# Performance work log

Hardware: AMD Instinct MI355X
Metric: run time of the kernel (lower is better)

## Reference

```python
import jax, jax.numpy as jnp
import numpy as np


def setup_inputs() -> dict:
    key = jax.random.key(0)
    ks = jax.random.split(key, 8)
    B, C, H, W = 4, 512, 64, 64
    O = 64  # output_size for f/g projections
    x = jax.random.normal(ks[0], (B, C, H, W), dtype=jnp.float32)
    s = 0.02
    f_w = jax.random.normal(ks[1], (O, C), dtype=jnp.float32) * s
    f_b = jnp.zeros((O,), dtype=jnp.float32)
    g_w = jax.random.normal(ks[2], (O, C), dtype=jnp.float32) * s
    g_b = jnp.zeros((O,), dtype=jnp.float32)
    h_w = jax.random.normal(ks[3], (C, C), dtype=jnp.float32) * s
    h_b = jnp.zeros((C,), dtype=jnp.float32)
    gamma = jnp.float32(0.5)  # torch init is 0.0; nonzero to exercise the attention path
    return {"x": x, "f_w": f_w, "f_b": f_b, "g_w": g_w, "g_b": g_b,
            "h_w": h_w, "h_b": h_b, "gamma": gamma}


def reference(x, f_w, f_b, g_w, g_b, h_w, h_b, gamma):
    B, C, Hh, Ww = x.shape
    N = Hh * Ww
    # 1x1 convs == per-pixel linear projections
    xf = x.reshape(B, C, N)                                   # [B,C,N]
    f = jnp.einsum('oc,bcn->bon', f_w, xf) + f_b[None, :, None]  # [B,O,N]
    g = jnp.einsum('oc,bcn->bon', g_w, xf) + g_b[None, :, None]  # [B,O,N]
    h = jnp.einsum('oc,bcn->bon', h_w, xf) + h_b[None, :, None]  # [B,C,N]
    # scores[b,i,j] = <f[:, i], g[:, j]>  (f transposed to [B,N,O] then bmm with g)
    scores = jnp.einsum('boi,boj->bij', f, g)                 # [B,N,N]
    # NOTE: original uses nn.Softmax(dim=1) -> normalize over the i (first N) axis
    sm = jax.nn.softmax(scores, axis=1)                       # [B,N,N]
    attn = jnp.einsum('bcn,bnm->bcm', h, sm)                  # [B,C,N]
    out = gamma * attn.reshape(B, C, Hh, Ww) + x
    return out
```

## Files before the change

### kernel.cpp

```cpp
#include <hip/hip_runtime.h>


#define N_PIX 4096
#define C_IN  512

typedef __attribute__((ext_vector_type(8)))  short bf16x8;
typedef __attribute__((ext_vector_type(16))) float f32x16;

typedef __attribute__((address_space(1))) const unsigned int guint;
typedef __attribute__((address_space(3))) unsigned int luint;

__device__ __forceinline__ void gload_lds16(const void* g, void* l) {
    __builtin_amdgcn_global_load_lds((guint*)g, (luint*)l, 16, 0, 0);
}

__device__ inline unsigned int f2bf(float f) {
    union { float f; unsigned u; } x; x.f = f;
    unsigned r = x.u + 0x7FFFu + ((x.u >> 16) & 1u);
    return r >> 16;
}

__device__ __forceinline__ unsigned cvt_pk_bf16(float a, float b) {
#if __has_builtin(__builtin_amdgcn_cvt_pk_bf16_f32)
    auto r = __builtin_amdgcn_cvt_pk_bf16_f32(a, b);
    unsigned u; __builtin_memcpy(&u, &r, 4); return u;
#else
    return f2bf(a) | (f2bf(b) << 16);
#endif
}

__device__ __forceinline__ unsigned pk_fp8x4(float a, float b, float c, float d) {
    int v = 0;
    v = __builtin_amdgcn_cvt_pk_fp8_f32(a, b, v, false);
    v = __builtin_amdgcn_cvt_pk_fp8_f32(c, d, v, true);
    return (unsigned)v;
}

__global__ __launch_bounds__(256) void pack_w(
    const float* __restrict__ f_w, const float* __restrict__ g_w,
    const float* __restrict__ h_w, unsigned short* __restrict__ wall)
{
    __shared__ __align__(16) unsigned short Ls[32 * 520];
    const int t  = threadIdx.x;
    const int tt = blockIdx.x;
    const float* W; int rbase;
    if (tt < 2)      { W = f_w; rbase = tt * 32; }
    else if (tt < 4) { W = g_w; rbase = (tt - 2) * 32; }
    else             { W = h_w; rbase = (tt - 4) * 32; }

    #pragma unroll
    for (int k = 0; k < 16; ++k) {
        const int off = (t + k * 256) * 4;
        const int row = off >> 9, col = off & 511;
        float4 v = *(const float4*)&W[(size_t)(rbase + row) * C_IN + col];
        uint2 pk; pk.x = cvt_pk_bf16(v.x, v.y); pk.y = cvt_pk_bf16(v.z, v.w);
        *(uint2*)&Ls[row * 520 + col] = pk;
    }
    __syncthreads();
    #pragma unroll
    for (int j = 0; j < 8; ++j) {
        const int o = t + j * 256;
        const int q = o >> 6, lq = o & 63;
        const int row = lq & 31, c0 = q * 16 + (lq >> 5) * 8;
        uint4 pk = *(const uint4*)&Ls[row * 520 + c0];
        *(uint4*)&wall[(size_t)tt * 16384 + (size_t)o * 8] = pk;
    }
}

__global__ __launch_bounds__(512, 4) void proj_kernel(
    const float* __restrict__ x,
    const unsigned short* __restrict__ wall,
    const float* __restrict__ f_b, const float* __restrict__ g_b,
    const float* __restrict__ h_b,
    unsigned short* __restrict__ fa, unsigned short* __restrict__ gbuf,
    unsigned char* __restrict__ ha)
{
    __shared__ __align__(16) unsigned short Xf[2][8192];
    const int t    = threadIdx.x;
    const int w    = t >> 6;
    const int l    = t & 63;
    const int half = l >> 5;
    const int tx = t & 15;
    const int ty = t >> 4;
    const int c0 = ty * 2;
    const int qs = c0 >> 4;
    const int woff = (c0 & 7);
    const int hfs = (c0 >> 3) & 1;

    const int blk = blockIdx.x;

    if (blk < 256) {
        const int b  = blk >> 6;
        const int nb = blk & 63;
        const int n0g = nb * 64;
        const int n0 = tx * 4;

        f32x16 acc[2][2];
        #pragma unroll
        for (int j = 0; j < 2; ++j)
            #pragma unroll
            for (int s = 0; s < 2; ++s)
                #pragma unroll
                for (int r = 0; r < 16; ++r) acc[j][s][r] = 0.f;

        const unsigned short* wp0 = wall + (size_t)(4 + w * 2) * 16384 + (size_t)l * 8;
        const unsigned short* wp1 = wp0 + 16384;
        bf16x8 wc0 = *(const bf16x8*)wp0;
        bf16x8 wc1 = *(const bf16x8*)wp1;

        float4 v0 = *(const float4*)&x[((size_t)(b * C_IN + c0)) * N_PIX + n0g + n0];
        float4 v1 = *(const float4*)&x[((size_t)(b * C_IN + c0 + 1)) * N_PIX + n0g + n0];

        for (int it = 0; it < 8; ++it) {
            {
                unsigned short* xb = &Xf[it & 1][0];
                const float a0[4] = {v0.x, v0.y, v0.z, v0.w};
                const float a1[4] = {v1.x, v1.y, v1.z, v1.w};
                #pragma unroll
                for (int j = 0; j < 4; ++j) {
                    const int n = n0 + j;
                    const int off = ((n >> 5) * 4 + qs) * 512
                                  + ((n & 31) + 32 * hfs) * 8 + woff;
                    *(unsigned*)&xb[off] = cvt_pk_bf16(a0[j], a1[j]);
                }
            }
            if (it < 7) {
                v0 = *(const float4*)&x[((size_t)(b * C_IN + (it + 1) * 64 + c0)) * N_PIX + n0g + n0];
                v1 = *(const float4*)&x[((size_t)(b * C_IN + (it + 1) * 64 + c0 + 1)) * N_PIX + n0g + n0];
            }
            __syncthreads();
            const unsigned short* xb = &Xf[it & 1][0];
            #pragma unroll
            for (int q = 0; q < 4; ++q) {
                const int qn = (it * 4 + q + 1) & 31;
                bf16x8 wn0 = *(const bf16x8*)(wp0 + (size_t)qn * 512);
                bf16x8 wn1 = *(const bf16x8*)(wp1 + (size_t)qn * 512);
                bf16x8 x0 = *(const bf16x8*)&xb[(0 * 4 + q) * 512 + l * 8];
                bf16x8 x1 = *(const bf16x8*)&xb[(1 * 4 + q) * 512 + l * 8];
                acc[0][0] = __builtin_amdgcn_mfma_f32_32x32x16_bf16(x0, wc0, acc[0][0], 0, 0, 0);
                acc[0][1] = __builtin_amdgcn_mfma_f32_32x32x16_bf16(x1, wc0, acc[0][1], 0, 0, 0);
                acc[1][0] = __builtin_amdgcn_mfma_f32_32x32x16_bf16(x0, wc1, acc[1][0], 0, 0, 0);
                acc[1][1] = __builtin_amdgcn_mfma_f32_32x32x16_bf16(x1, wc1, acc[1][1], 0, 0, 0);
                wc0 = wn0; wc1 = wn1;
            }
            __syncthreads();
        }

        #pragma unroll
        for (int j = 0; j < 2; ++j) {
            const int ctile = w * 2 + j;
            const float hb = h_b[ctile * 32 + (l & 31)];
            #pragma unroll
            for (int ns = 0; ns < 2; ++ns) {
                const int ntile = nb * 2 + ns;
                #pragma unroll
                for (int j2 = 0; j2 < 4; ++j2) {
                    const int q  = ntile * 2 + (j2 >> 1);
                    const int lp = (l & 31) + 32 * (j2 & 1);
                    unsigned pk = pk_fp8x4(acc[j][ns][4 * j2 + 0] + hb,
                                           acc[j][ns][4 * j2 + 1] + hb,
                                           acc[j][ns][4 * j2 + 2] + hb,
                                           acc[j][ns][4 * j2 + 3] + hb);
                    size_t off = (((size_t)(b * 16 + ctile) * 256 + q) * 64 + lp) * 8 + 4 * half;
                    *(unsigned*)&ha[off] = pk;
                }
            }
        }
    } else {
        const int blk2 = blk - 256;
        const int b   = blk2 >> 5;
        const int nb2 = blk2 & 31;
        const int n0g = nb2 * 128;
        const int tt    = w & 3;
        const int npair = w >> 2;

        f32x16 acc[2];
        #pragma unroll
        for (int s = 0; s < 2; ++s)
            #pragma unroll
            for (int r = 0; r < 16; ++r) acc[s][r] = 0.f;

        const unsigned short* wpf = wall + (size_t)tt * 16384 + (size_t)l * 8;
        bf16x8 wcf = *(const bf16x8*)wpf;

        float4 v00 = *(const float4*)&x[((size_t)(b * C_IN + c0)) * N_PIX + n0g + tx * 4];
        float4 v10 = *(const float4*)&x[((size_t)(b * C_IN + c0 + 1)) * N_PIX + n0g + tx * 4];
        float4 v01 = *(const float4*)&x[((size_t)(b * C_IN + c0)) * N_PIX + n0g + 64 + tx * 4];
        float4 v11 = *(const float4*)&x[((size_t)(b * C_IN + c0 + 1)) * N_PIX + n0g + 64 + tx * 4];

        for (int it = 0; it < 8; ++it) {
            {
                unsigned short* xb = &Xf[it & 1][0];
                const float a00[4] = {v00.x, v00.y, v00.z, v00.w};
                const float a10[4] = {v10.x, v10.y, v10.z, v10.w};
                const float a01[4] = {v01.x, v01.y, v01.z, v01.w};
                const float a11[4] = {v11.x, v11.y, v11.z, v11.w};
                #pragma unroll
                for (int j = 0; j < 4; ++j) {
                    const int n = tx * 4 + j;
                    const int off0 = ((n >> 5) * 4 + qs) * 512
                                   + ((n & 31) + 32 * hfs) * 8 + woff;
                    *(unsigned*)&xb[off0] = cvt_pk_bf16(a00[j], a10[j]);
                    const int n2 = 64 + n;
                    const int off1 = ((n2 >> 5) * 4 + qs) * 512
                                   + ((n2 & 31) + 32 * hfs) * 8 + woff;
                    *(unsigned*)&xb[off1] = cvt_pk_bf16(a01[j], a11[j]);
                }
            }
            if (it < 7) {
                const size_t rb = (size_t)(b * C_IN + (it + 1) * 64 + c0) * N_PIX + n0g;
                v00 = *(const float4*)&x[rb + tx * 4];
                v10 = *(const float4*)&x[rb + N_PIX + tx * 4];
                v01 = *(const float4*)&x[rb + 64 + tx * 4];
                v11 = *(const float4*)&x[rb + N_PIX + 64 + tx * 4];
            }
            __syncthreads();
            const unsigned short* xb = &Xf[it & 1][0];
            #pragma unroll
            for (int q = 0; q < 4; ++q) {
                const int qn = (it * 4 + q + 1) & 31;
                bf16x8 wnf = *(const bf16x8*)(wpf + (size_t)qn * 512);
                bf16x8 x0 = *(const bf16x8*)&xb[((npair * 2 + 0) * 4 + q) * 512 + l * 8];
                bf16x8 x1 = *(const bf16x8*)&xb[((npair * 2 + 1) * 4 + q) * 512 + l * 8];
                acc[0] = __builtin_amdgcn_mfma_f32_32x32x16_bf16(wcf, x0, acc[0], 0, 0, 0);
                acc[1] = __builtin_amdgcn_mfma_f32_32x32x16_bf16(wcf, x1, acc[1], 0, 0, 0);
                wcf = wnf;
            }
            __syncthreads();
        }

        unsigned short* buf = (tt < 2) ? fa : gbuf;
        const float* bias = (tt < 2) ? f_b : g_b;
        #pragma unroll
        for (int s = 0; s < 2; ++s) {
            const int ntile = nb2 * 4 + npair * 2 + s;
            #pragma unroll
            for (int j2 = 0; j2 < 4; ++j2) {
                const int o_base = (tt & 1) * 32 + 8 * j2 + 4 * half;
                float4 bv = *(const float4*)&bias[o_base];
                const int q  = o_base >> 4;
                const int lp = (l & 31) + 32 * (j2 & 1);
                uint2 pk;
                pk.x = cvt_pk_bf16(acc[s][4 * j2 + 0] + bv.x, acc[s][4 * j2 + 1] + bv.y);
                pk.y = cvt_pk_bf16(acc[s][4 * j2 + 2] + bv.z, acc[s][4 * j2 + 3] + bv.w);
                size_t off = (((size_t)(b * 128 + ntile) * 4 + q) * 64 + lp) * 8 + 4 * half;
                *(uint2*)&buf[off] = pk;
            }
        }
    }
}

__global__ __launch_bounds__(512, 4) void attn_kernel(
    const unsigned short* __restrict__ fa,
    const unsigned short* __restrict__ gbuf,
    const unsigned char* __restrict__ ha,
    const float* __restrict__ x,
    const float* __restrict__ gamma_p,
    float* __restrict__ out)
{
    __shared__ unsigned char Ebuf[2][64 * 136];
    __shared__ __align__(16) unsigned short Fst[2][16 * 512];
    __shared__ float den_part[4][64];
    __shared__ float den_inv[64];

    const int t    = threadIdx.x;
    const int w    = t >> 6;
    const int l    = t & 63;
    const int lane = l & 31;
    const int half = l >> 5;
    const int nsub = w & 3;
    const int mt   = w >> 2;

    const int blk   = blockIdx.x;
    const int chalf = blk & 1;
    const int b     = (blk >> 1) & 3;
    const int mi    = blk >> 3;
    const int m0    = mi * 64;

    bf16x8 gfrag[4];
    {
        const unsigned short* gp = gbuf
            + ((size_t)(b * 128 + mi * 2 + mt) * 4) * 512 + (size_t)l * 8;
        #pragma unroll
        for (int q = 0; q < 4; ++q)
            gfrag[q] = *(const bf16x8*)(gp + (size_t)q * 512);
    }

    f32x16 acc[2];
    #pragma unroll
    for (int j = 0; j < 2; ++j)
        #pragma unroll
        for (int r = 0; r < 16; ++r) acc[j][r] = 0.f;

    float denp = 0.f;

    const unsigned short* fbase = fa + (size_t)b * (128 * 4) * 512;
    const int ctg = chalf * 8 + w;
    const unsigned char* hbase = ha + ((size_t)(b * 16 + ctg)) * 256 * 512 + (size_t)l * 8;

    #pragma unroll
    for (int j = 0; j < 2; ++j) {
        const int chunk = w * 2 + j;
        const unsigned short* src = fbase
            + ((size_t)((chunk >> 2)) * 4 + (chunk & 3)) * 512 + (size_t)l * 8;
        gload_lds16(src, &Fst[0][chunk * 512]);
    }
    __syncthreads();

    for (int nt = 0; nt < 32; ++nt) {
        if (nt < 31) {
            #pragma unroll
            for (int j = 0; j < 2; ++j) {
                const int chunk = w * 2 + j;
                const unsigned short* src = fbase
                    + ((size_t)((nt + 1) * 4 + (chunk >> 2)) * 4 + (chunk & 3)) * 512
                    + (size_t)l * 8;
                gload_lds16(src, &Fst[(nt + 1) & 1][chunk * 512]);
            }
        }
        bf16x8 ff[4];
        #pragma unroll
        for (int q = 0; q < 4; ++q)
            ff[q] = *(const bf16x8*)&Fst[nt & 1][(nsub * 4 + q) * 512 + l * 8];
        f32x16 s;
        #pragma unroll
        for (int r = 0; r < 16; ++r) s[r] = 0.f;
        #pragma unroll
        for (int q = 0; q < 4; ++q)
            s = __builtin_amdgcn_mfma_f32_32x32x16_bf16(ff[q], gfrag[q], s, 0, 0, 0);
        unsigned char* ew = &Ebuf[nt & 1][(mt * 32 + lane) * 136 + nsub * 32 + half * 4];
        #pragma unroll
        for (int r4 = 0; r4 < 4; ++r4) {
            float e0 = __expf(fminf(s[r4 * 4 + 0] - 6.0f, 6.0f));
            float e1 = __expf(fminf(s[r4 * 4 + 1] - 6.0f, 6.0f));
            float e2 = __expf(fminf(s[r4 * 4 + 2] - 6.0f, 6.0f));
            float e3 = __expf(fminf(s[r4 * 4 + 3] - 6.0f, 6.0f));
            denp += (e0 + e1) + (e2 + e3);
            *(unsigned*)(ew + r4 * 8) = pk_fp8x4(e0, e1, e2, e3);
        }
        long hreg[8];
        {
            const unsigned char* hp = hbase + (size_t)(nt * 8) * 512;
            #pragma unroll
            for (int q = 0; q < 8; ++q)
                hreg[q] = *(const long*)(hp + (size_t)q * 512);
        }
        __syncthreads();
        const unsigned char* eb = &Ebuf[nt & 1][0];
        #pragma unroll
        for (int q = 0; q < 8; ++q) {
            long b0 = *(const long*)(eb + lane * 136 + q * 16 + half * 8);
            long b1 = *(const long*)(eb + (32 + lane) * 136 + q * 16 + half * 8);
            acc[0] = __builtin_amdgcn_mfma_f32_32x32x16_fp8_fp8(hreg[q], b0, acc[0], 0, 0, 0);
            acc[1] = __builtin_amdgcn_mfma_f32_32x32x16_fp8_fp8(hreg[q], b1, acc[1], 0, 0, 0);
        }
    }

    denp += __shfl_xor(denp, 32, 64);
    if (l < 32) den_part[nsub][mt * 32 + lane] = denp;
    __syncthreads();
    if (t < 64) {
        float d = den_part[0][t] + den_part[1][t] + den_part[2][t] + den_part[3][t];
        den_inv[t] = 1.0f / d;
    }
    __syncthreads();

    const float gs = gamma_p[0];
    #pragma unroll
    for (int mt2 = 0; mt2 < 2; ++mt2) {
        const int mloc = mt2 * 32 + lane;
        const float dinv = den_inv[mloc];
        const int m = m0 + mloc;
        #pragma unroll
        for (int r = 0; r < 16; ++r) {
            const int c = ctg * 32 + (r & 3) + ((r >> 2) * 8) + half * 4;
            const size_t idx = ((size_t)(b * C_IN + c)) * N_PIX + m;
            out[idx] = gs * acc[mt2][r] * dinv + x[idx];
        }
    }
}

extern "C" void kernel_launch(void* const* d_in, const int* in_sizes, int n_in,
                              void* d_out, int out_size, void* d_ws, size_t ws_size,
                              hipStream_t stream)
{
    const float* x     = (const float*)d_in[0];
    const float* f_w   = (const float*)d_in[1];
    const float* f_b   = (const float*)d_in[2];
    const float* g_w   = (const float*)d_in[3];
    const float* g_b   = (const float*)d_in[4];
    const float* h_w   = (const float*)d_in[5];
    const float* h_b   = (const float*)d_in[6];
    const float* gamma = (const float*)d_in[7];
    float* out = (float*)d_out;

    unsigned short* fa   = (unsigned short*)d_ws;
    unsigned short* gbuf = fa + (1u << 20);
    unsigned char*  ha   = (unsigned char*)(gbuf + (1u << 20));
    unsigned short* wall = (unsigned short*)(ha + (8u << 20));

    pack_w<<<20, 256, 0, stream>>>(f_w, g_w, h_w, wall);

    proj_kernel<<<384, 512, 0, stream>>>(x, wall, f_b, g_b, h_b, fa, gbuf, ha);

    attn_kernel<<<512, 512, 0, stream>>>(fa, gbuf, ha, x, gamma, out);
}
```

Baseline: 185.7 us.

## Use MI355 scaled 32x32x64 FP8 MFMA for attention-value product with row-major H

The H-times-softmax product now uses the gfx950 mfma_scale 32x32x64 f8f6f4 instruction with unit scales, in place of eight 32x32x16 fp8 MFMAs per tile. To feed it, the fp8 H projection output moves from a pre-swizzled fragment layout to plain channel-major rows. Each lane then loads two contiguous 32-byte vectors per step instead of eight scattered 8-byte loads. The aim is fewer MFMA issues and wider, more coalesced H loads. The cost is more LDS reads per MFMA for the E operand, and the projection kernel now writes H with strided rows.

```diff
diff --git a/kernel.cpp b/kernel.cpp
--- a/kernel.cpp
+++ b/kernel.cpp
@@ -6,6 +6,7 @@
 
 typedef __attribute__((ext_vector_type(8)))  short bf16x8;
 typedef __attribute__((ext_vector_type(16))) float f32x16;
+typedef __attribute__((ext_vector_type(8)))  int   i32x8;
 
 typedef __attribute__((address_space(1))) const unsigned int guint;
 typedef __attribute__((address_space(3))) unsigned int luint;
@@ -149,20 +150,18 @@
         #pragma unroll
         for (int j = 0; j < 2; ++j) {
             const int ctile = w * 2 + j;
-            const float hb = h_b[ctile * 32 + (l & 31)];
+            const int ch = ctile * 32 + (l & 31);
+            const float hb = h_b[ch];
+            unsigned char* hrow = ha + ((size_t)(b * C_IN + ch)) * N_PIX + n0g + 4 * half;
             #pragma unroll
             for (int ns = 0; ns < 2; ++ns) {
-                const int ntile = nb * 2 + ns;
                 #pragma unroll
                 for (int j2 = 0; j2 < 4; ++j2) {
-                    const int q  = ntile * 2 + (j2 >> 1);
-                    const int lp = (l & 31) + 32 * (j2 & 1);
                     unsigned pk = pk_fp8x4(acc[j][ns][4 * j2 + 0] + hb,
                                            acc[j][ns][4 * j2 + 1] + hb,
                                            acc[j][ns][4 * j2 + 2] + hb,
                                            acc[j][ns][4 * j2 + 3] + hb);
-                    size_t off = (((size_t)(b * 16 + ctile) * 256 + q) * 64 + lp) * 8 + 4 * half;
-                    *(unsigned*)&ha[off] = pk;
+                    *(unsigned*)&hrow[ns * 32 + j2 * 8] = pk;
                 }
             }
         }
@@ -258,7 +257,7 @@
     const float* __restrict__ gamma_p,
     float* __restrict__ out)
 {
-    __shared__ unsigned char Ebuf[2][64 * 136];
+    __shared__ __align__(16) unsigned char Ebuf[2][64 * 136];
     __shared__ __align__(16) unsigned short Fst[2][16 * 512];
     __shared__ float den_part[4][64];
     __shared__ float den_inv[64];
@@ -296,7 +295,8 @@
 
     const unsigned short* fbase = fa + (size_t)b * (128 * 4) * 512;
     const int ctg = chalf * 8 + w;
-    const unsigned char* hbase = ha + ((size_t)(b * 16 + ctg)) * 256 * 512 + (size_t)l * 8;
+    const unsigned char* hbase = ha
+        + ((size_t)(b * C_IN + ctg * 32 + lane)) * N_PIX + (size_t)half * 32;
 
     #pragma unroll
     for (int j = 0; j < 2; ++j) {
@@ -338,21 +338,28 @@
             denp += (e0 + e1) + (e2 + e3);
             *(unsigned*)(ew + r4 * 8) = pk_fp8x4(e0, e1, e2, e3);
         }
-        long hreg[8];
+        i32x8 a0, a1;
         {
-            const unsigned char* hp = hbase + (size_t)(nt * 8) * 512;
-            #pragma unroll
-            for (int q = 0; q < 8; ++q)
-                hreg[q] = *(const long*)(hp + (size_t)q * 512);
+            const unsigned char* hp = hbase + (size_t)nt * 128;
+            a0 = *(const i32x8*)hp;
+            a1 = *(const i32x8*)(hp + 64);
         }
         __syncthreads();
         const unsigned char* eb = &Ebuf[nt & 1][0];
         #pragma unroll
-        for (int q = 0; q < 8; ++q) {
-            long b0 = *(const long*)(eb + lane * 136 + q * 16 + half * 8);
-            long b1 = *(const long*)(eb + (32 + lane) * 136 + q * 16 + half * 8);
-            acc[0] = __builtin_amdgcn_mfma_f32_32x32x16_fp8_fp8(hreg[q], b0, acc[0], 0, 0, 0);
-            acc[1] = __builtin_amdgcn_mfma_f32_32x32x16_fp8_fp8(hreg[q], b1, acc[1], 0, 0, 0);
+        for (int kt = 0; kt < 2; ++kt) {
+            const unsigned char* e0 = eb + lane * 136 + kt * 64 + half * 32;
+            union { i32x8 v; long d[4]; } b0, b1;
+            #pragma unroll
+            for (int j = 0; j < 4; ++j) {
+                b0.d[j] = *(const long*)(e0 + 8 * j);
+                b1.d[j] = *(const long*)(e0 + 32 * 136 + 8 * j);
+            }
+            const i32x8 av = kt ? a1 : a0;
+            acc[0] = __builtin_amdgcn_mfma_scale_f32_32x32x64_f8f6f4(
+                av, b0.v, acc[0], 0, 0, 0, 127, 0, 127);
+            acc[1] = __builtin_amdgcn_mfma_scale_f32_32x32x64_f8f6f4(
+                av, b1.v, acc[1], 0, 0, 0, 127, 0, 127);
         }
     }
 
```

Result: no change. 187.5 us (+1.0%).
